# Performance work log

Measured on AMD Instinct MI355X. Metric: run time of the kernel, lower is better.

Reference implementation:

```python
import jax, jax.numpy as jnp
import numpy as np

N_NODES = 50000
N_EDGES = 800000
HID = 64
NUM_CURR = 15
NUM_PAY = 7
CURR_DIM = 8
PAY_DIM = 4
NUM_NUM = 5
EDGE_REPR = 2 * HID + 2 * CURR_DIM + PAY_DIM + NUM_NUM  # 153


def setup_inputs() -> dict:
    key = jax.random.key(0)
    ks = jax.random.split(key, 24)
    f = lambda k, shape, scale=0.05: jax.random.normal(k, shape, jnp.float32) * scale
    inp = {
        'node_feats': jax.random.normal(ks[0], (N_NODES, 2), jnp.float32),
        'src': jax.random.randint(ks[1], (N_EDGES,), 0, N_NODES, jnp.int32),
        'dst': jax.random.randint(ks[2], (N_EDGES,), 0, N_NODES, jnp.int32),
        'payment_currency': jax.random.randint(ks[3], (N_EDGES,), 0, NUM_CURR, jnp.int32),
        'receiving_currency': jax.random.randint(ks[4], (N_EDGES,), 0, NUM_CURR, jnp.int32),
        'payment_format': jax.random.randint(ks[5], (N_EDGES,), 0, NUM_PAY, jnp.int32),
        'numericals': jax.random.normal(ks[6], (N_EDGES, NUM_NUM), jnp.float32),
        # GCN layer params
        'W0': f(ks[7], (2, HID)), 'b0': f(ks[8], (HID,)),
        'W1': f(ks[9], (HID, HID)), 'b1': f(ks[10], (HID,)),
        'W2': f(ks[11], (HID, HID)), 'b2': f(ks[12], (HID,)),
        # edge embeddings
        'curr_emb': f(ks[13], (NUM_CURR, CURR_DIM), 1.0),
        'pay_emb': f(ks[14], (NUM_PAY, PAY_DIM), 1.0),
        # edge classifier MLP
        'M0': f(ks[15], (EDGE_REPR, HID)), 'bM0': f(ks[16], (HID,)),
        'M1': f(ks[17], (HID, HID)), 'bM1': f(ks[18], (HID,)),
        'M2': f(ks[19], (HID, 2)), 'bM2': f(ks[20], (2,)),
    }
    return inp


def reference(node_feats, src, dst, payment_currency, receiving_currency,
              payment_format, numericals, W0, b0, W1, b1, W2, b2,
              curr_emb, pay_emb, M0, bM0, M1, bM1, M2, bM2):
    # symmetric-ish GCN norm: deg^{-1/2} on source (message) and dest (after sum)
    ones = jnp.ones((src.shape[0],), jnp.float32)
    deg = jax.ops.segment_sum(ones, dst, num_segments=N_NODES)
    norm = jnp.clip(deg, 1.0, None) ** -0.5  # [N]
    norm = norm[:, None]

    def gcn(h, W, b, residual):
        Wh = h @ W + b                         # [N, HID]
        m = Wh[src] * norm[src]                # gather-scale per edge [E, HID]
        agg = jax.ops.segment_sum(m, dst, num_segments=N_NODES)  # scatter-sum
        out = jax.nn.relu(agg * norm)
        return out + h if residual else out    # res_linear is Identity (dims match)

    h = gcn(node_feats, W0, b0, False)
    h = gcn(h, W1, b1, True)
    h = gcn(h, W2, b2, True)
    # dropout is inference no-op

    edge_repr = jnp.concatenate([
        h[src], h[dst],
        curr_emb[payment_currency], curr_emb[receiving_currency],
        pay_emb[payment_format], numericals,
    ], axis=1)  # [E, 153]

    x = jax.nn.relu(edge_repr @ M0 + bM0)
    x = jax.nn.relu(x @ M1 + bM1)
    logits = x @ M2 + bM2  # [E, 2]
    return logits
```

## Files before the change

### kernel.cpp

```cpp
#include <hip/hip_runtime.h>
#include <hip/hip_bf16.h>

#define N_NODES 50000
#define N_EDGES 800000
#define HID 64

typedef __attribute__((ext_vector_type(2))) float f32x2;

__device__ __forceinline__ unsigned short f2bf(float f) {
    union { float f; unsigned int i; } v;
    v.f = f;
    unsigned int b = v.i;
    return (unsigned short)((b + 0x7FFFu + ((b >> 16) & 1u)) >> 16);
}

__device__ __forceinline__ float bf2f(unsigned short u) {
    union { unsigned int i; float f; } t;
    t.i = ((unsigned int)u) << 16;
    return t.f;
}

__device__ __forceinline__ f32x2 bfpair(unsigned int u) {
    union { unsigned int i; float f; } lo, hi;
    lo.i = u << 16;
    hi.i = u & 0xFFFF0000u;
    f32x2 r;
    r[0] = lo.f;
    r[1] = hi.f;
    return r;
}


__global__ void k_deg(const int* __restrict__ dst, int* __restrict__ deg, int n) {
    int e = blockIdx.x * blockDim.x + threadIdx.x;
    if (e < n) atomicAdd(&deg[dst[e]], 1);
}

__global__ void k_off(const int* __restrict__ deg, int* __restrict__ row_ptr,
                      int* __restrict__ cursor, float* __restrict__ norm,
                      int* __restrict__ gcount, int n) {
    int i = blockIdx.x * blockDim.x + threadIdx.x;
    int lane = threadIdx.x & 63;
    int v = (i < n) ? deg[i] : 0;
    int s = v;
#pragma unroll
    for (int off = 1; off < 64; off <<= 1) {
        int t = __shfl_up(s, off);
        if (lane >= off) s += t;
    }
    int total = __shfl(s, 63);
    int base = 0;
    if (lane == 63) base = atomicAdd(gcount, total);
    base = __shfl(base, 63);
    int ex = base + s - v;
    if (i < n) {
        row_ptr[i] = ex;
        cursor[i]  = ex;
        norm[i] = 1.0f / sqrtf(fmaxf((float)v, 1.0f));
    }
}

__global__ void k_scatter(const int* __restrict__ src, const int* __restrict__ dst,
                          int* __restrict__ cursor, int* __restrict__ csr_src, int n) {
    int e = blockIdx.x * blockDim.x + threadIdx.x;
    if (e < n) {
        int d = dst[e];
        int pos = atomicAdd(&cursor[d], 1);
        csr_src[pos] = src[e];
    }
}


__global__ __launch_bounds__(256) void k_l0(const float2* __restrict__ nf,
                                            const float* __restrict__ norm,
                                            const int* __restrict__ row_ptr,
                                            const int* __restrict__ deg,
                                            const int* __restrict__ csr_src,
                                            const float* __restrict__ W0,
                                            const float* __restrict__ b0,
                                            float* __restrict__ h,
                                            unsigned short* __restrict__ hn,
                                            float* __restrict__ snorm, int n_nodes) {
    int lane = threadIdx.x & 63, wid = threadIdx.x >> 6;
    int n = blockIdx.x * 4 + wid;
    if (n >= n_nodes) return;
    int r0 = row_ptr[n], dc = deg[n];
    float a0 = 0.f, a1 = 0.f, sn = 0.f;
    for (int i = lane; i < dc; i += 64) {
        int s = csr_src[r0 + i];
        float ns = norm[s];
        float2 v = nf[s];
        a0 += v.x * ns;
        a1 += v.y * ns;
        sn += ns;
    }
#pragma unroll
    for (int off = 32; off; off >>= 1) {
        a0 += __shfl_xor(a0, off);
        a1 += __shfl_xor(a1, off);
        sn += __shfl_xor(sn, off);
    }
    float nn = norm[n];
    float v = (a0 * W0[lane] + a1 * W0[64 + lane] + b0[lane] * sn) * nn;
    v = fmaxf(v, 0.f);
    h[(size_t)n * 64 + lane] = v;
    hn[(size_t)n * 64 + lane] = f2bf(v * nn);
    if (lane == 0) snorm[n] = sn;
}


__global__ __launch_bounds__(256) void k_agg(const unsigned short* __restrict__ hn,
                                             const int* __restrict__ row_ptr,
                                             const int* __restrict__ deg,
                                             const int* __restrict__ csr_src,
                                             float* __restrict__ g, int n_nodes) {
    int lane = threadIdx.x & 63, wid = threadIdx.x >> 6;
    int n = blockIdx.x * 4 + wid;
    if (n >= n_nodes) return;
    int r0 = row_ptr[n], dc = deg[n];
    float acc = 0.f;
    int i = 0;
    for (; i + 4 <= dc; i += 4) {
        int s0 = csr_src[r0 + i + 0];
        int s1 = csr_src[r0 + i + 1];
        int s2 = csr_src[r0 + i + 2];
        int s3 = csr_src[r0 + i + 3];
        float v0 = bf2f(hn[(size_t)s0 * 64 + lane]);
        float v1 = bf2f(hn[(size_t)s1 * 64 + lane]);
        float v2 = bf2f(hn[(size_t)s2 * 64 + lane]);
        float v3 = bf2f(hn[(size_t)s3 * 64 + lane]);
        acc += (v0 + v1) + (v2 + v3);
    }
    for (; i < dc; ++i) acc += bf2f(hn[(size_t)csr_src[r0 + i] * 64 + lane]);
    g[(size_t)n * 64 + lane] = acc;
}


__global__ __launch_bounds__(256) void k_mv(const float* __restrict__ g,
                                            const float* __restrict__ h_in,
                                            const float* __restrict__ W,
                                            const float* __restrict__ b,
                                            const float* __restrict__ norm,
                                            const float* __restrict__ snorm,
                                            float* __restrict__ h_out,
                                            unsigned short* __restrict__ hn_out, int n_nodes) {
    int lane = threadIdx.x & 63, wid = threadIdx.x >> 6;
    int n = blockIdx.x * 64 + lane;
    if (n >= n_nodes) return;
    const int j0 = wid * 16;
    float sn = snorm[n];
    float y[16];
    const float* bj = b + j0;
#pragma unroll
    for (int q = 0; q < 16; ++q) y[q] = bj[q] * sn;
    const float4* g4 = (const float4*)(g + (size_t)n * 64);
    const float* Wj = W + j0;
#pragma unroll
    for (int k4 = 0; k4 < 16; ++k4) {
        float4 xv = g4[k4];
        const float* w0 = Wj + (k4 * 4 + 0) * 64;
        const float* w1 = Wj + (k4 * 4 + 1) * 64;
        const float* w2 = Wj + (k4 * 4 + 2) * 64;
        const float* w3 = Wj + (k4 * 4 + 3) * 64;
#pragma unroll
        for (int q = 0; q < 16; ++q) {
            y[q] = fmaf(xv.x, w0[q], y[q]);
            y[q] = fmaf(xv.y, w1[q], y[q]);
            y[q] = fmaf(xv.z, w2[q], y[q]);
            y[q] = fmaf(xv.w, w3[q], y[q]);
        }
    }
    float nn = norm[n];
    const float4* h4 = (const float4*)(h_in + (size_t)n * 64 + j0);
    float4* o4 = (float4*)(h_out + (size_t)n * 64 + j0);
    float ov[16];
#pragma unroll
    for (int q4 = 0; q4 < 4; ++q4) {
        float4 hv = h4[q4];
        float4 o;
        o.x = fmaxf(y[q4*4+0] * nn, 0.f) + hv.x;
        o.y = fmaxf(y[q4*4+1] * nn, 0.f) + hv.y;
        o.z = fmaxf(y[q4*4+2] * nn, 0.f) + hv.z;
        o.w = fmaxf(y[q4*4+3] * nn, 0.f) + hv.w;
        o4[q4] = o;
        ov[q4*4+0] = o.x; ov[q4*4+1] = o.y; ov[q4*4+2] = o.z; ov[q4*4+3] = o.w;
    }
    if (hn_out) {
        uint4* s4 = (uint4*)(hn_out + (size_t)n * 64 + j0);
#pragma unroll
        for (int q8 = 0; q8 < 2; ++q8) {
            uint4 w;
            w.x = (unsigned int)f2bf(ov[q8*8+0] * nn) | ((unsigned int)f2bf(ov[q8*8+1] * nn) << 16);
            w.y = (unsigned int)f2bf(ov[q8*8+2] * nn) | ((unsigned int)f2bf(ov[q8*8+3] * nn) << 16);
            w.z = (unsigned int)f2bf(ov[q8*8+4] * nn) | ((unsigned int)f2bf(ov[q8*8+5] * nn) << 16);
            w.w = (unsigned int)f2bf(ov[q8*8+6] * nn) | ((unsigned int)f2bf(ov[q8*8+7] * nn) << 16);
            s4[q8] = w;
        }
    }
}


__global__ __launch_bounds__(512) void k_mv2(const float* __restrict__ h,
                                             const float* __restrict__ M0,
                                             unsigned short* __restrict__ Ab,
                                             unsigned short* __restrict__ Bb,
                                             int n_nodes) {
    int lane = threadIdx.x & 63, wid = threadIdx.x >> 6;
    int n = blockIdx.x * 64 + lane;
    if (n >= n_nodes) return;
    const int tbl = wid >> 2;
    const int j0 = (wid & 3) * 16;
    float y[16];
#pragma unroll
    for (int q = 0; q < 16; ++q) y[q] = 0.f;
    const float4* h4 = (const float4*)(h + (size_t)n * 64);
    const float* Wj = M0 + tbl * 4096 + j0;
#pragma unroll
    for (int k4 = 0; k4 < 16; ++k4) {
        float4 xv = h4[k4];
        const float* w0 = Wj + (k4 * 4 + 0) * 64;
        const float* w1 = Wj + (k4 * 4 + 1) * 64;
        const float* w2 = Wj + (k4 * 4 + 2) * 64;
        const float* w3 = Wj + (k4 * 4 + 3) * 64;
#pragma unroll
        for (int q = 0; q < 16; ++q) {
            y[q] = fmaf(xv.x, w0[q], y[q]);
            y[q] = fmaf(xv.y, w1[q], y[q]);
            y[q] = fmaf(xv.z, w2[q], y[q]);
            y[q] = fmaf(xv.w, w3[q], y[q]);
        }
    }
    unsigned short* Ot = (tbl ? Bb : Ab) + (size_t)n * 64 + j0;
    uint4* o4 = (uint4*)Ot;
#pragma unroll
    for (int q = 0; q < 2; ++q) {
        uint4 ov;
        ov.x = (unsigned int)f2bf(y[q*8+0]) | ((unsigned int)f2bf(y[q*8+1]) << 16);
        ov.y = (unsigned int)f2bf(y[q*8+2]) | ((unsigned int)f2bf(y[q*8+3]) << 16);
        ov.z = (unsigned int)f2bf(y[q*8+4]) | ((unsigned int)f2bf(y[q*8+5]) << 16);
        ov.w = (unsigned int)f2bf(y[q*8+6]) | ((unsigned int)f2bf(y[q*8+7]) << 16);
        o4[q] = ov;
    }
}


__global__ void k_small(const float* __restrict__ curr_emb, const float* __restrict__ pay_emb,
                        const float* __restrict__ M0, float* __restrict__ C1,
                        float* __restrict__ C2, float* __restrict__ P) {
    int tid = threadIdx.x;
    for (int idx = tid; idx < 15 * 64; idx += blockDim.x) {
        int c = idx >> 6, j = idx & 63;
        float s1 = 0.f, s2 = 0.f;
        for (int k = 0; k < 8; ++k) {
            float ce = curr_emb[c * 8 + k];
            s1 += ce * M0[(128 + k) * 64 + j];
            s2 += ce * M0[(136 + k) * 64 + j];
        }
        C1[idx] = s1;
        C2[idx] = s2;
    }
    for (int idx = tid; idx < 7 * 64; idx += blockDim.x) {
        int p = idx >> 6, j = idx & 63;
        float s = 0.f;
        for (int k = 0; k < 4; ++k) s += pay_emb[p * 4 + k] * M0[(144 + k) * 64 + j];
        P[idx] = s;
    }
}

__global__ void k_combo(const float* __restrict__ C1, const float* __restrict__ C2,
                        const float* __restrict__ P, const float* __restrict__ bM0,
                        float* __restrict__ T, int total) {
    int idx = blockIdx.x * blockDim.x + threadIdx.x;
    if (idx < total) {
        int j = idx & 63, c = idx >> 6;
        int p = c % 7, cc = c / 7;
        int c2 = cc % 15, c1 = cc / 15;
        T[idx] = C1[c1 * 64 + j] + C2[c2 * 64 + j] + P[p * 64 + j] + bM0[j];
    }
}


__global__ __launch_bounds__(256, 2) void k_edge(const unsigned short* __restrict__ Ab,
                                                 const unsigned short* __restrict__ Bb,
                                                 const float* __restrict__ T,
                                                 const float* __restrict__ M0,
                                                 const float* __restrict__ M1,
                                                 const float* __restrict__ bM1,
                                                 const float* __restrict__ M2,
                                                 const float* __restrict__ bM2,
                                                 const int* __restrict__ src,
                                                 const int* __restrict__ dst,
                                                 const int* __restrict__ pc,
                                                 const int* __restrict__ rc,
                                                 const int* __restrict__ pf,
                                                 const float* __restrict__ num,
                                                 float* __restrict__ out, int n_edges) {
    int e = blockIdx.x * blockDim.x + threadIdx.x;
    if (e >= n_edges) return;
    int s = src[e], d = dst[e];
    int combo = (pc[e] * 15 + rc[e]) * 7 + pf[e];
    float nk[5];
#pragma unroll
    for (int k = 0; k < 5; ++k) nk[k] = num[(size_t)e * 5 + k];

    f32x2 x0[32];
    const f32x2* t2 = (const f32x2*)(T + (size_t)combo * 64);
#pragma unroll
    for (int q = 0; q < 32; ++q) x0[q] = t2[q];

    const uint4* ra = (const uint4*)(Ab + (size_t)s * 64);
#pragma unroll
    for (int q = 0; q < 8; ++q) {
        uint4 v = ra[q];
        x0[q*4+0] += bfpair(v.x);
        x0[q*4+1] += bfpair(v.y);
        x0[q*4+2] += bfpair(v.z);
        x0[q*4+3] += bfpair(v.w);
    }
    const uint4* rb = (const uint4*)(Bb + (size_t)d * 64);
#pragma unroll
    for (int q = 0; q < 8; ++q) {
        uint4 v = rb[q];
        x0[q*4+0] += bfpair(v.x);
        x0[q*4+1] += bfpair(v.y);
        x0[q*4+2] += bfpair(v.z);
        x0[q*4+3] += bfpair(v.w);
    }
#pragma unroll
    for (int k = 0; k < 5; ++k) {
        const f32x2* mp = (const f32x2*)(M0 + (148 + k) * 64);
        f32x2 nv;
        nv[0] = nk[k]; nv[1] = nk[k];
#pragma unroll
        for (int q = 0; q < 32; ++q) x0[q] = __builtin_elementwise_fma(nv, mp[q], x0[q]);
    }
    f32x2 zero2;
    zero2[0] = 0.f; zero2[1] = 0.f;
#pragma unroll
    for (int q = 0; q < 32; ++q) x0[q] = __builtin_elementwise_max(x0[q], zero2);

    float lg0 = bM2[0], lg1 = bM2[1];
#pragma unroll
    for (int jh = 0; jh < 2; ++jh) {
        f32x2 x1[16];
        const f32x2* bb = (const f32x2*)(bM1 + jh * 32);
#pragma unroll
        for (int q = 0; q < 16; ++q) x1[q] = bb[q];
#pragma unroll
        for (int k = 0; k < 64; ++k) {
            float xk = x0[k >> 1][k & 1];
            f32x2 xv;
            xv[0] = xk; xv[1] = xk;
            const f32x2* mr = (const f32x2*)(M1 + k * 64 + jh * 32);
#pragma unroll
            for (int q = 0; q < 16; ++q) x1[q] = __builtin_elementwise_fma(xv, mr[q], x1[q]);
        }
#pragma unroll
        for (int q = 0; q < 16; ++q) {
            f32x2 xv = __builtin_elementwise_max(x1[q], zero2);
            int j = jh * 32 + q * 2;
            lg0 = fmaf(xv[0], M2[j * 2 + 0], lg0);
            lg1 = fmaf(xv[0], M2[j * 2 + 1], lg1);
            lg0 = fmaf(xv[1], M2[j * 2 + 2], lg0);
            lg1 = fmaf(xv[1], M2[j * 2 + 3], lg1);
        }
    }
    ((float2*)out)[e] = make_float2(lg0, lg1);
}


extern "C" void kernel_launch(void* const* d_in, const int* in_sizes, int n_in,
                              void* d_out, int out_size, void* d_ws, size_t ws_size,
                              hipStream_t stream) {
    const float2* node_feats = (const float2*)d_in[0];
    const int*   src  = (const int*)d_in[1];
    const int*   dst  = (const int*)d_in[2];
    const int*   pc   = (const int*)d_in[3];
    const int*   rc   = (const int*)d_in[4];
    const int*   pf   = (const int*)d_in[5];
    const float* num  = (const float*)d_in[6];
    const float* W0   = (const float*)d_in[7];
    const float* b0   = (const float*)d_in[8];
    const float* W1   = (const float*)d_in[9];
    const float* b1   = (const float*)d_in[10];
    const float* W2   = (const float*)d_in[11];
    const float* b2   = (const float*)d_in[12];
    const float* curr_emb = (const float*)d_in[13];
    const float* pay_emb  = (const float*)d_in[14];
    const float* M0   = (const float*)d_in[15];
    const float* bM0  = (const float*)d_in[16];
    const float* M1   = (const float*)d_in[17];
    const float* bM1  = (const float*)d_in[18];
    const float* M2   = (const float*)d_in[19];
    const float* bM2  = (const float*)d_in[20];
    float* out = (float*)d_out;

    char* w = (char*)d_ws;
    auto alloc = [&](size_t bytes) {
        char* p = w;
        w += (bytes + 255) & ~size_t(255);
        return p;
    };
    int*    deg     = (int*)alloc(N_NODES * 4);
    int*    gcount  = (int*)alloc(256);
    float*  norm    = (float*)alloc(N_NODES * 4);
    float*  snorm   = (float*)alloc(N_NODES * 4);
    int*    row_ptr = (int*)alloc((N_NODES + 1) * 4);
    int*    cursor  = (int*)alloc(N_NODES * 4);
    int*    csr_src = (int*)alloc(N_EDGES * 4);
    float*  B1      = (float*)alloc(N_NODES * HID * 4);
    unsigned short* B2 = (unsigned short*)alloc(N_NODES * HID * 2);
    float*  B3      = (float*)alloc(N_NODES * HID * 4);
    float*  B4      = (float*)alloc(N_NODES * HID * 4);
    unsigned short* Ab = (unsigned short*)alloc(N_NODES * HID * 2);
    unsigned short* Bb = (unsigned short*)alloc(N_NODES * HID * 2);
    float*  C1      = (float*)alloc(15 * 64 * 4);
    float*  C2      = (float*)alloc(15 * 64 * 4);
    float*  P       = (float*)alloc(7 * 64 * 4);
    float*  T       = (float*)alloc(15 * 15 * 7 * 64 * 4);

    hipMemsetAsync(deg, 0, N_NODES * 4, stream);
    hipMemsetAsync(gcount, 0, 256, stream);
    k_deg<<<(N_EDGES + 255) / 256, 256, 0, stream>>>(dst, deg, N_EDGES);
    k_off<<<(N_NODES + 255) / 256, 256, 0, stream>>>(deg, row_ptr, cursor, norm, gcount, N_NODES);
    k_scatter<<<(N_EDGES + 255) / 256, 256, 0, stream>>>(src, dst, cursor, csr_src, N_EDGES);
    k_l0<<<(N_NODES + 3) / 4, 256, 0, stream>>>(node_feats, norm, row_ptr, deg, csr_src,
                                                W0, b0, B1, B2, snorm, N_NODES);
    k_agg<<<(N_NODES + 3) / 4, 256, 0, stream>>>(B2, row_ptr, deg, csr_src, B3, N_NODES);
    k_mv<<<(N_NODES + 63) / 64, 256, 0, stream>>>(B3, B1, W1, b1, norm, snorm, B4, B2, N_NODES);
    k_agg<<<(N_NODES + 3) / 4, 256, 0, stream>>>(B2, row_ptr, deg, csr_src, B3, N_NODES);
    k_mv<<<(N_NODES + 63) / 64, 256, 0, stream>>>(B3, B4, W2, b2, norm, snorm, B1, nullptr, N_NODES);
    k_small<<<1, 256, 0, stream>>>(curr_emb, pay_emb, M0, C1, C2, P);
    k_combo<<<(15 * 15 * 7 * 64 + 255) / 256, 256, 0, stream>>>(C1, C2, P, bM0, T, 15 * 15 * 7 * 64);
    k_mv2<<<(N_NODES + 63) / 64, 512, 0, stream>>>(B1, M0, Ab, Bb, N_NODES);
    k_edge<<<(N_EDGES + 255) / 256, 256, 0, stream>>>(Ab, Bb, T, M0, M1, bM1, M2, bM2,
                                                      src, dst, pc, rc, pf, num, out, N_EDGES);
}
```

Measured before the change: 602.3 us.

## Fuse M0 node projection into last GCN matvec, pair-wise agg, merge table kernels

The final GCN layer's k_mv now also projects its output through the two M0 node blocks, staging the row in shared memory. This removes the separate k_mv2 kernel and the fp32 write and re-read of the final h. k_small and k_combo are merged into one k_tab kernel that builds the categorical lookup table directly. k_agg now reads packed bf16 pairs, with each half-wave handling alternate neighbours, and combines the halves with a shuffle. The cost is extra register and LDS pressure in k_mv plus a block-wide barrier.

```diff
diff --git a/kernel.cpp b/kernel.cpp
--- a/kernel.cpp
+++ b/kernel.cpp
@@ -28,6 +28,10 @@
     r[0] = lo.f;
     r[1] = hi.f;
     return r;
+}
+
+__device__ __forceinline__ unsigned int pkbf(f32x2 v) {
+    return (unsigned int)f2bf(v[0]) | ((unsigned int)f2bf(v[1]) << 16);
 }
 
 
@@ -117,22 +121,30 @@
     int lane = threadIdx.x & 63, wid = threadIdx.x >> 6;
     int n = blockIdx.x * 4 + wid;
     if (n >= n_nodes) return;
+    const unsigned int* hnu = (const unsigned int*)hn;
     int r0 = row_ptr[n], dc = deg[n];
-    float acc = 0.f;
+    int half = lane >> 5;
+    int fl = lane & 31;
+    f32x2 acc;
+    acc[0] = 0.f; acc[1] = 0.f;
     int i = 0;
     for (; i + 4 <= dc; i += 4) {
-        int s0 = csr_src[r0 + i + 0];
-        int s1 = csr_src[r0 + i + 1];
-        int s2 = csr_src[r0 + i + 2];
-        int s3 = csr_src[r0 + i + 3];
-        float v0 = bf2f(hn[(size_t)s0 * 64 + lane]);
-        float v1 = bf2f(hn[(size_t)s1 * 64 + lane]);
-        float v2 = bf2f(hn[(size_t)s2 * 64 + lane]);
-        float v3 = bf2f(hn[(size_t)s3 * 64 + lane]);
-        acc += (v0 + v1) + (v2 + v3);
-    }
-    for (; i < dc; ++i) acc += bf2f(hn[(size_t)csr_src[r0 + i] * 64 + lane]);
-    g[(size_t)n * 64 + lane] = acc;
+        int s0 = csr_src[r0 + i + half];
+        int s1 = csr_src[r0 + i + 2 + half];
+        acc += bfpair(hnu[(size_t)s0 * 32 + fl]);
+        acc += bfpair(hnu[(size_t)s1 * 32 + fl]);
+    }
+    for (; i + 2 <= dc; i += 2) {
+        int s0 = csr_src[r0 + i + half];
+        acc += bfpair(hnu[(size_t)s0 * 32 + fl]);
+    }
+    if (i < dc && half == 0) {
+        int s0 = csr_src[r0 + i];
+        acc += bfpair(hnu[(size_t)s0 * 32 + fl]);
+    }
+    acc[0] += __shfl_xor(acc[0], 32);
+    acc[1] += __shfl_xor(acc[1], 32);
+    if (half == 0) ((float2*)g)[(size_t)n * 32 + fl] = make_float2(acc[0], acc[1]);
 }
 
 
@@ -143,140 +155,120 @@
                                             const float* __restrict__ norm,
                                             const float* __restrict__ snorm,
                                             float* __restrict__ h_out,
-                                            unsigned short* __restrict__ hn_out, int n_nodes) {
+                                            unsigned short* __restrict__ hn_out,
+                                            unsigned short* __restrict__ Ab,
+                                            unsigned short* __restrict__ Bb,
+                                            const float* __restrict__ M0, int n_nodes) {
+    __shared__ float xs[64][65];
     int lane = threadIdx.x & 63, wid = threadIdx.x >> 6;
     int n = blockIdx.x * 64 + lane;
-    if (n >= n_nodes) return;
+    bool act = n < n_nodes;
     const int j0 = wid * 16;
-    float sn = snorm[n];
-    float y[16];
-    const float* bj = b + j0;
-#pragma unroll
-    for (int q = 0; q < 16; ++q) y[q] = bj[q] * sn;
-    const float4* g4 = (const float4*)(g + (size_t)n * 64);
-    const float* Wj = W + j0;
-#pragma unroll
-    for (int k4 = 0; k4 < 16; ++k4) {
-        float4 xv = g4[k4];
-        const float* w0 = Wj + (k4 * 4 + 0) * 64;
-        const float* w1 = Wj + (k4 * 4 + 1) * 64;
-        const float* w2 = Wj + (k4 * 4 + 2) * 64;
-        const float* w3 = Wj + (k4 * 4 + 3) * 64;
-#pragma unroll
-        for (int q = 0; q < 16; ++q) {
-            y[q] = fmaf(xv.x, w0[q], y[q]);
-            y[q] = fmaf(xv.y, w1[q], y[q]);
-            y[q] = fmaf(xv.z, w2[q], y[q]);
-            y[q] = fmaf(xv.w, w3[q], y[q]);
-        }
-    }
-    float nn = norm[n];
-    const float4* h4 = (const float4*)(h_in + (size_t)n * 64 + j0);
-    float4* o4 = (float4*)(h_out + (size_t)n * 64 + j0);
     float ov[16];
-#pragma unroll
-    for (int q4 = 0; q4 < 4; ++q4) {
-        float4 hv = h4[q4];
-        float4 o;
-        o.x = fmaxf(y[q4*4+0] * nn, 0.f) + hv.x;
-        o.y = fmaxf(y[q4*4+1] * nn, 0.f) + hv.y;
-        o.z = fmaxf(y[q4*4+2] * nn, 0.f) + hv.z;
-        o.w = fmaxf(y[q4*4+3] * nn, 0.f) + hv.w;
-        o4[q4] = o;
-        ov[q4*4+0] = o.x; ov[q4*4+1] = o.y; ov[q4*4+2] = o.z; ov[q4*4+3] = o.w;
-    }
-    if (hn_out) {
-        uint4* s4 = (uint4*)(hn_out + (size_t)n * 64 + j0);
-#pragma unroll
-        for (int q8 = 0; q8 < 2; ++q8) {
-            uint4 w;
-            w.x = (unsigned int)f2bf(ov[q8*8+0] * nn) | ((unsigned int)f2bf(ov[q8*8+1] * nn) << 16);
-            w.y = (unsigned int)f2bf(ov[q8*8+2] * nn) | ((unsigned int)f2bf(ov[q8*8+3] * nn) << 16);
-            w.z = (unsigned int)f2bf(ov[q8*8+4] * nn) | ((unsigned int)f2bf(ov[q8*8+5] * nn) << 16);
-            w.w = (unsigned int)f2bf(ov[q8*8+6] * nn) | ((unsigned int)f2bf(ov[q8*8+7] * nn) << 16);
-            s4[q8] = w;
-        }
-    }
-}
-
-
-__global__ __launch_bounds__(512) void k_mv2(const float* __restrict__ h,
-                                             const float* __restrict__ M0,
-                                             unsigned short* __restrict__ Ab,
-                                             unsigned short* __restrict__ Bb,
-                                             int n_nodes) {
-    int lane = threadIdx.x & 63, wid = threadIdx.x >> 6;
-    int n = blockIdx.x * 64 + lane;
-    if (n >= n_nodes) return;
-    const int tbl = wid >> 2;
-    const int j0 = (wid & 3) * 16;
-    float y[16];
-#pragma unroll
-    for (int q = 0; q < 16; ++q) y[q] = 0.f;
-    const float4* h4 = (const float4*)(h + (size_t)n * 64);
-    const float* Wj = M0 + tbl * 4096 + j0;
-#pragma unroll
-    for (int k4 = 0; k4 < 16; ++k4) {
-        float4 xv = h4[k4];
-        const float* w0 = Wj + (k4 * 4 + 0) * 64;
-        const float* w1 = Wj + (k4 * 4 + 1) * 64;
-        const float* w2 = Wj + (k4 * 4 + 2) * 64;
-        const float* w3 = Wj + (k4 * 4 + 3) * 64;
-#pragma unroll
-        for (int q = 0; q < 16; ++q) {
-            y[q] = fmaf(xv.x, w0[q], y[q]);
-            y[q] = fmaf(xv.y, w1[q], y[q]);
-            y[q] = fmaf(xv.z, w2[q], y[q]);
-            y[q] = fmaf(xv.w, w3[q], y[q]);
-        }
-    }
-    unsigned short* Ot = (tbl ? Bb : Ab) + (size_t)n * 64 + j0;
-    uint4* o4 = (uint4*)Ot;
-#pragma unroll
-    for (int q = 0; q < 2; ++q) {
-        uint4 ov;
-        ov.x = (unsigned int)f2bf(y[q*8+0]) | ((unsigned int)f2bf(y[q*8+1]) << 16);
-        ov.y = (unsigned int)f2bf(y[q*8+2]) | ((unsigned int)f2bf(y[q*8+3]) << 16);
-        ov.z = (unsigned int)f2bf(y[q*8+4]) | ((unsigned int)f2bf(y[q*8+5]) << 16);
-        ov.w = (unsigned int)f2bf(y[q*8+6]) | ((unsigned int)f2bf(y[q*8+7]) << 16);
-        o4[q] = ov;
-    }
-}
-
-
-__global__ void k_small(const float* __restrict__ curr_emb, const float* __restrict__ pay_emb,
-                        const float* __restrict__ M0, float* __restrict__ C1,
-                        float* __restrict__ C2, float* __restrict__ P) {
-    int tid = threadIdx.x;
-    for (int idx = tid; idx < 15 * 64; idx += blockDim.x) {
-        int c = idx >> 6, j = idx & 63;
-        float s1 = 0.f, s2 = 0.f;
-        for (int k = 0; k < 8; ++k) {
-            float ce = curr_emb[c * 8 + k];
-            s1 += ce * M0[(128 + k) * 64 + j];
-            s2 += ce * M0[(136 + k) * 64 + j];
-        }
-        C1[idx] = s1;
-        C2[idx] = s2;
-    }
-    for (int idx = tid; idx < 7 * 64; idx += blockDim.x) {
-        int p = idx >> 6, j = idx & 63;
-        float s = 0.f;
-        for (int k = 0; k < 4; ++k) s += pay_emb[p * 4 + k] * M0[(144 + k) * 64 + j];
-        P[idx] = s;
-    }
-}
-
-__global__ void k_combo(const float* __restrict__ C1, const float* __restrict__ C2,
-                        const float* __restrict__ P, const float* __restrict__ bM0,
-                        float* __restrict__ T, int total) {
+    if (act) {
+        float sn = snorm[n];
+        float y[16];
+        const float* bj = b + j0;
+#pragma unroll
+        for (int q = 0; q < 16; ++q) y[q] = bj[q] * sn;
+        const float4* g4 = (const float4*)(g + (size_t)n * 64);
+        const float* Wj = W + j0;
+#pragma unroll
+        for (int k4 = 0; k4 < 16; ++k4) {
+            float4 xv = g4[k4];
+            const float* w0 = Wj + (k4 * 4 + 0) * 64;
+            const float* w1 = Wj + (k4 * 4 + 1) * 64;
+            const float* w2 = Wj + (k4 * 4 + 2) * 64;
+            const float* w3 = Wj + (k4 * 4 + 3) * 64;
+#pragma unroll
+            for (int q = 0; q < 16; ++q) {
+                y[q] = fmaf(xv.x, w0[q], y[q]);
+                y[q] = fmaf(xv.y, w1[q], y[q]);
+                y[q] = fmaf(xv.z, w2[q], y[q]);
+                y[q] = fmaf(xv.w, w3[q], y[q]);
+            }
+        }
+        float nn = norm[n];
+        const float* hme = h_in + (size_t)n * 64 + j0;
+#pragma unroll
+        for (int q = 0; q < 16; ++q) ov[q] = fmaxf(y[q] * nn, 0.f) + hme[q];
+        if (h_out) {
+            float4* o4 = (float4*)(h_out + (size_t)n * 64 + j0);
+#pragma unroll
+            for (int q4 = 0; q4 < 4; ++q4) {
+                float4 o;
+                o.x = ov[q4*4+0]; o.y = ov[q4*4+1]; o.z = ov[q4*4+2]; o.w = ov[q4*4+3];
+                o4[q4] = o;
+            }
+        }
+        if (hn_out) {
+            uint4* s4 = (uint4*)(hn_out + (size_t)n * 64 + j0);
+#pragma unroll
+            for (int q8 = 0; q8 < 2; ++q8) {
+                uint4 w;
+                w.x = (unsigned int)f2bf(ov[q8*8+0] * nn) | ((unsigned int)f2bf(ov[q8*8+1] * nn) << 16);
+                w.y = (unsigned int)f2bf(ov[q8*8+2] * nn) | ((unsigned int)f2bf(ov[q8*8+3] * nn) << 16);
+                w.z = (unsigned int)f2bf(ov[q8*8+4] * nn) | ((unsigned int)f2bf(ov[q8*8+5] * nn) << 16);
+                w.w = (unsigned int)f2bf(ov[q8*8+6] * nn) | ((unsigned int)f2bf(ov[q8*8+7] * nn) << 16);
+                s4[q8] = w;
+            }
+        }
+    }
+    if (Ab) {
+        if (act) {
+#pragma unroll
+            for (int q = 0; q < 16; ++q) xs[lane][j0 + q] = ov[q];
+        }
+        __syncthreads();
+        if (act) {
+            f32x2 ya[8], yb[8];
+#pragma unroll
+            for (int q = 0; q < 8; ++q) { ya[q][0] = 0.f; ya[q][1] = 0.f; yb[q][0] = 0.f; yb[q][1] = 0.f; }
+#pragma unroll
+            for (int k = 0; k < 64; ++k) {
+                float xk = xs[lane][k];
+                f32x2 xk2;
+                xk2[0] = xk; xk2[1] = xk;
+                const f32x2* wa = (const f32x2*)(M0 + k * 64 + j0);
+                const f32x2* wb = (const f32x2*)(M0 + 4096 + k * 64 + j0);
+#pragma unroll
+                for (int q = 0; q < 8; ++q) {
+                    ya[q] = __builtin_elementwise_fma(xk2, wa[q], ya[q]);
+                    yb[q] = __builtin_elementwise_fma(xk2, wb[q], yb[q]);
+                }
+            }
+            uint4* pA = (uint4*)(Ab + (size_t)n * 64 + j0);
+            uint4* pB = (uint4*)(Bb + (size_t)n * 64 + j0);
+            uint4 wa4, wb4;
+            wa4.x = pkbf(ya[0]); wa4.y = pkbf(ya[1]); wa4.z = pkbf(ya[2]); wa4.w = pkbf(ya[3]);
+            pA[0] = wa4;
+            wa4.x = pkbf(ya[4]); wa4.y = pkbf(ya[5]); wa4.z = pkbf(ya[6]); wa4.w = pkbf(ya[7]);
+            pA[1] = wa4;
+            wb4.x = pkbf(yb[0]); wb4.y = pkbf(yb[1]); wb4.z = pkbf(yb[2]); wb4.w = pkbf(yb[3]);
+            pB[0] = wb4;
+            wb4.x = pkbf(yb[4]); wb4.y = pkbf(yb[5]); wb4.z = pkbf(yb[6]); wb4.w = pkbf(yb[7]);
+            pB[1] = wb4;
+        }
+    }
+}
+
+
+__global__ void k_tab(const float* __restrict__ curr_emb, const float* __restrict__ pay_emb,
+                      const float* __restrict__ M0, const float* __restrict__ bM0,
+                      float* __restrict__ T, int total) {
     int idx = blockIdx.x * blockDim.x + threadIdx.x;
-    if (idx < total) {
-        int j = idx & 63, c = idx >> 6;
-        int p = c % 7, cc = c / 7;
-        int c2 = cc % 15, c1 = cc / 15;
-        T[idx] = C1[c1 * 64 + j] + C2[c2 * 64 + j] + P[p * 64 + j] + bM0[j];
-    }
+    if (idx >= total) return;
+    int j = idx & 63, c = idx >> 6;
+    int p = c % 7, cc = c / 7;
+    int c2 = cc % 15, c1 = cc / 15;
+    float s = bM0[j];
+#pragma unroll
+    for (int k = 0; k < 8; ++k) s = fmaf(curr_emb[c1 * 8 + k], M0[(128 + k) * 64 + j], s);
+#pragma unroll
+    for (int k = 0; k < 8; ++k) s = fmaf(curr_emb[c2 * 8 + k], M0[(136 + k) * 64 + j], s);
+#pragma unroll
+    for (int k = 0; k < 4; ++k) s = fmaf(pay_emb[p * 4 + k], M0[(144 + k) * 64 + j], s);
+    T[idx] = s;
 }
 
 
@@ -414,9 +406,6 @@
     float*  B4      = (float*)alloc(N_NODES * HID * 4);
     unsigned short* Ab = (unsigned short*)alloc(N_NODES * HID * 2);
     unsigned short* Bb = (unsigned short*)alloc(N_NODES * HID * 2);
-    float*  C1      = (float*)alloc(15 * 64 * 4);
-    float*  C2      = (float*)alloc(15 * 64 * 4);
-    float*  P       = (float*)alloc(7 * 64 * 4);
     float*  T       = (float*)alloc(15 * 15 * 7 * 64 * 4);
 
     hipMemsetAsync(deg, 0, N_NODES * 4, stream);
@@ -427,12 +416,13 @@
     k_l0<<<(N_NODES + 3) / 4, 256, 0, stream>>>(node_feats, norm, row_ptr, deg, csr_src,
                                                 W0, b0, B1, B2, snorm, N_NODES);
     k_agg<<<(N_NODES + 3) / 4, 256, 0, stream>>>(B2, row_ptr, deg, csr_src, B3, N_NODES);
-    k_mv<<<(N_NODES + 63) / 64, 256, 0, stream>>>(B3, B1, W1, b1, norm, snorm, B4, B2, N_NODES);
+    k_mv<<<(N_NODES + 63) / 64, 256, 0, stream>>>(B3, B1, W1, b1, norm, snorm,
+                                                  B4, B2, nullptr, nullptr, nullptr, N_NODES);
     k_agg<<<(N_NODES + 3) / 4, 256, 0, stream>>>(B2, row_ptr, deg, csr_src, B3, N_NODES);
-    k_mv<<<(N_NODES + 63) / 64, 256, 0, stream>>>(B3, B4, W2, b2, norm, snorm, B1, nullptr, N_NODES);
-    k_small<<<1, 256, 0, stream>>>(curr_emb, pay_emb, M0, C1, C2, P);
-    k_combo<<<(15 * 15 * 7 * 64 + 255) / 256, 256, 0, stream>>>(C1, C2, P, bM0, T, 15 * 15 * 7 * 64);
-    k_mv2<<<(N_NODES + 63) / 64, 512, 0, stream>>>(B1, M0, Ab, Bb, N_NODES);
+    k_mv<<<(N_NODES + 63) / 64, 256, 0, stream>>>(B3, B4, W2, b2, norm, snorm,
+                                                  nullptr, nullptr, Ab, Bb, M0, N_NODES);
+    k_tab<<<(15 * 15 * 7 * 64 + 255) / 256, 256, 0, stream>>>(curr_emb, pay_emb, M0, bM0,
+                                                              T, 15 * 15 * 7 * 64);
     k_edge<<<(N_EDGES + 255) / 256, 256, 0, stream>>>(Ab, Bb, T, M0, M1, bM1, M2, bM2,
                                                       src, dst, pc, rc, pf, num, out, N_EDGES);
 }
```

Result: faster. 570.6 us (-5.3%).
